# Kernel optimization log

Hardware: AMD Instinct MI355X
Metric: run time of the kernel (lower is better)

## Reference

```python
import jax, jax.numpy as jnp
import numpy as np

# Fixed intrinsics from PhotometricLoss.__init__
W, H = 640, 480
FU, FV = 320.0, 320.0
CU, CV = (W - 1) / 2.0, (H - 1) / 2.0  # cu,cv default to (dim-1)/2
BASELINE = 0.25  # t_vec = [0.25, 0, 0], r_mat = I


def _grid_sample_bilinear_zeros(img, grid):
    """torch.F.grid_sample(img, grid) with bilinear interp, zeros padding,
    align_corners=False (modern torch default).
    img: [B,C,H,W], grid: [B,H,W,2] (x,y) in [-1,1]. Returns [B,C,H,W]."""
    B, C, Hh, Ww = img.shape
    gx, gy = grid[..., 0], grid[..., 1]
    # unnormalize (align_corners=False)
    x = ((gx + 1.0) * Ww - 1.0) * 0.5
    y = ((gy + 1.0) * Hh - 1.0) * 0.5
    x0 = jnp.floor(x)
    y0 = jnp.floor(y)
    wx1 = x - x0
    wy1 = y - y0
    wx0 = 1.0 - wx1
    wy0 = 1.0 - wy1
    b = jnp.arange(B)[:, None, None]

    def gather(yi, xi):
        valid = (xi >= 0) & (xi < Ww) & (yi >= 0) & (yi < Hh)
        xi_c = jnp.clip(xi, 0, Ww - 1).astype(jnp.int32)
        yi_c = jnp.clip(yi, 0, Hh - 1).astype(jnp.int32)
        v = img[b, :, yi_c, xi_c]  # [B,H,W,C]
        return v * valid[..., None].astype(img.dtype)

    out = (gather(y0, x0) * (wy0 * wx0)[..., None]
           + gather(y0, x0 + 1) * (wy0 * wx1)[..., None]
           + gather(y0 + 1, x0) * (wy1 * wx0)[..., None]
           + gather(y0 + 1, x0 + 1) * (wy1 * wx1)[..., None])
    return jnp.transpose(out, (0, 3, 1, 2))  # [B,C,H,W]


def setup_inputs() -> dict:
    key = jax.random.key(0)
    k1, k2, k3 = jax.random.split(key, 3)
    Bsz = 32
    rgb_right = jax.random.uniform(k1, (Bsz, 3, H, W), jnp.float32) * 255.0
    rgb_left = jax.random.uniform(k2, (Bsz, 3, H, W), jnp.float32) * 255.0
    # depth in [1, 80] meters -> disparity fu*B/Z in [1, 80] pixels
    depth_right = jax.random.uniform(k3, (Bsz, 1, H, W), jnp.float32) * 79.0 + 1.0
    return {"rgb_right": rgb_right, "rgb_left": rgb_left, "depth_right": depth_right}


def reference(rgb_right, rgb_left, depth_right):
    # camera rays (X_cam, Y_cam) from Intrinsics
    u = jnp.arange(W, dtype=jnp.float32)
    v = jnp.arange(H, dtype=jnp.float32)
    X_cam = (u[None, :] - CU) / FU  # [1,W] -> broadcasts over H
    Y_cam = (v[:, None] - CV) / FV  # [H,1]

    d = depth_right[:, 0]  # [B,H,W]
    # image_to_pointcloud + transform_curr_to_near (R = I, t = [BASELINE,0,0])
    X = d * X_cam + BASELINE
    Y = d * Y_cam
    Z = jnp.maximum(d, 0.001)  # clamp(min=0.001)

    # pointcloud_to_image
    U_proj = FU * X / Z + CU
    V_proj = FV * Y / Z + CV
    un = 2.0 * U_proj / (W - 1) - 1.0
    vn = 2.0 * V_proj / (H - 1) - 1.0
    un = jnp.where(jnp.abs(un) > 1.0, 2.0, un)  # out-of-frame -> 2 (zeros padding)
    vn = jnp.where(jnp.abs(vn) > 1.0, 2.0, vn)
    grid = jnp.stack([un, vn], axis=-1)  # [B,H,W,2]

    warped = _grid_sample_bilinear_zeros(rgb_left, grid)  # [B,3,H,W]

    diff = jnp.sum(jnp.abs(warped - rgb_right), axis=1)  # [B,H,W]
    valid_mask = ((jnp.sum(warped, axis=1) > 0)
                  & (jnp.sum(rgb_left, axis=1) > 0)).astype(diff.dtype)
    return jnp.mean(diff * valid_mask)
```

## Files before the change

### kernel.cpp

```cpp
#include <hip/hip_runtime.h>

#define IMG_W 640
#define IMG_H 480
#define BATCH 32
#define HWSZ (IMG_H * IMG_W)
#define CHWSZ (3 * HWSZ)
#define NPIX (BATCH * HWSZ)

#define NROWS (BATCH * IMG_H)
#define NTHREADS 320

__global__ __launch_bounds__(NTHREADS) void photo_main(
    const float* __restrict__ rgb_right,
    const float* __restrict__ rgb_left,
    const float* __restrict__ depth,
    float* __restrict__ partials)
{
    const int rowid = blockIdx.x;
    const int b = rowid / IMG_H;
    const int v = rowid - b * IMG_H;

    const float yrow = (480.0f * (float)v) / 479.0f - 0.5f;
    const int y0s = (int)floorf(yrow);
    const int r0 = min(max(y0s, 0), IMG_H - 1);
    const int r1 = min(max(y0s + 1, 0), IMG_H - 1);

    __shared__ float lds[2 * 3 * IMG_W];

    const float* __restrict__ Lb = rgb_left + (size_t)b * CHWSZ;

#pragma unroll
    for (int k = 0; k < 3; ++k) {
        const int idx = threadIdx.x + k * NTHREADS;
        const int rowch = idx / 160;
        const int x4 = idx - rowch * 160;
        const int rowsel = (rowch >= 3) ? 1 : 0;
        const int c = rowch - 3 * rowsel;
        const int rsrc = rowsel ? r1 : r0;
        const float4 val = *(const float4*)(Lb + (size_t)c * HWSZ + (size_t)rsrc * IMG_W + 4 * x4);
        *(float4*)(&lds[rowch * IMG_W + 4 * x4]) = val;
    }
    __syncthreads();

    const size_t dbase = (size_t)b * HWSZ + (size_t)v * IMG_W;
    const size_t rbase = (size_t)b * CHWSZ + (size_t)v * IMG_W;
    const float Yc = ((float)v - 239.5f) * (1.0f / 320.0f);

    float acc = 0.0f;

#pragma unroll
    for (int i = 0; i < 2; ++i) {
        const int u = threadIdx.x + i * NTHREADS;

        const float dd = depth[dbase + u];
        const float Rr = rgb_right[rbase + u];
        const float Rg = rgb_right[rbase + HWSZ + u];
        const float Rb2 = rgb_right[rbase + 2 * HWSZ + u];

        const float Xc = ((float)u - 319.5f) * (1.0f / 320.0f);
        const float X = dd * Xc + 0.25f;
        const float Y = dd * Yc;
        const float Z = fmaxf(dd, 0.001f);
        const float rz = __builtin_amdgcn_rcpf(Z);
        const float Up = 320.0f * X * rz + 319.5f;
        const float Vp = 320.0f * Y * rz + 239.5f;

        float un = 2.0f * Up * (1.0f / 639.0f) - 1.0f;
        float vn = 2.0f * Vp * (1.0f / 479.0f) - 1.0f;
        un = (fabsf(un) > 1.0f) ? 2.0f : un;
        vn = (fabsf(vn) > 1.0f) ? 2.0f : vn;

        const float x = ((un + 1.0f) * (float)IMG_W - 1.0f) * 0.5f;
        const float y = ((vn + 1.0f) * (float)IMG_H - 1.0f) * 0.5f;
        const float x0f = floorf(x);
        const float y0f = floorf(y);
        const float wx1 = x - x0f;
        const float wy1 = y - y0f;
        const float wx0 = 1.0f - wx1;
        const float wy0 = 1.0f - wy1;
        const int x0 = (int)x0f, y0 = (int)y0f;
        const int x1 = x0 + 1,   y1 = y0 + 1;

        const bool vx0 = (x0 >= 0) & (x0 < IMG_W);
        const bool vx1 = (x1 >= 0) & (x1 < IMG_W);
        const bool vy0 = (y0 >= 0) & (y0 < IMG_H);
        const bool vy1 = (y1 >= 0) & (y1 < IMG_H);
        const int cx0 = min(max(x0, 0), IMG_W - 1);
        const int cx1 = min(max(x1, 0), IMG_W - 1);

        const float w00 = wy0 * wx0 * ((vy0 & vx0) ? 1.0f : 0.0f);
        const float w01 = wy0 * wx1 * ((vy0 & vx1) ? 1.0f : 0.0f);
        const float w10 = wy1 * wx0 * ((vy1 & vx0) ? 1.0f : 0.0f);
        const float w11 = wy1 * wx1 * ((vy1 & vx1) ? 1.0f : 0.0f);

        const int s0 = min(max(y0 - y0s, 0), 1) * (3 * IMG_W);
        const int s1 = min(max(y1 - y0s, 0), 1) * (3 * IMG_W);

        float wsum = 0.0f;
        float diff = 0.0f;
#pragma unroll
        for (int c = 0; c < 3; ++c) {
            const int cb = c * IMG_W;
            const float t00 = lds[s0 + cb + cx0];
            const float t01 = lds[s0 + cb + cx1];
            const float t10 = lds[s1 + cb + cx0];
            const float t11 = lds[s1 + cb + cx1];
            const float w = w00 * t00 + w01 * t01 + w10 * t10 + w11 * t11;
            const float r = (c == 0) ? Rr : ((c == 1) ? Rg : Rb2);
            wsum += w;
            diff += fabsf(w - r);
        }

        acc += (wsum > 0.0f) ? diff : 0.0f;
    }

    for (int off = 32; off > 0; off >>= 1)
        acc += __shfl_down(acc, off, 64);

    __shared__ float red[NTHREADS / 64];
    const int lane = threadIdx.x & 63;
    const int wave = threadIdx.x >> 6;
    if (lane == 0) red[wave] = acc;
    __syncthreads();
    if (threadIdx.x == 0) {
        float s = 0.0f;
#pragma unroll
        for (int w = 0; w < NTHREADS / 64; ++w) s += red[w];
        partials[blockIdx.x] = s;
    }
}

__global__ __launch_bounds__(1024) void photo_finish(
    const float* __restrict__ partials,
    float* __restrict__ out,
    int nb)
{
    double s = 0.0;
    for (int i = threadIdx.x; i < nb; i += blockDim.x)
        s += (double)partials[i];

    for (int off = 32; off > 0; off >>= 1)
        s += __shfl_down(s, off, 64);

    __shared__ double lds[16];
    const int lane = threadIdx.x & 63;
    const int wave = threadIdx.x >> 6;
    if (lane == 0) lds[wave] = s;
    __syncthreads();
    if (threadIdx.x == 0) {
        double t = 0.0;
#pragma unroll
        for (int w = 0; w < 16; ++w) t += lds[w];
        out[0] = (float)(t / (double)NPIX);
    }
}

extern "C" void kernel_launch(void* const* d_in, const int* in_sizes, int n_in,
                              void* d_out, int out_size, void* d_ws, size_t ws_size,
                              hipStream_t stream) {
    const float* rgb_right = (const float*)d_in[0];
    const float* rgb_left  = (const float*)d_in[1];
    const float* depth     = (const float*)d_in[2];
    float* partials = (float*)d_ws;
    float* out = (float*)d_out;

    photo_main<<<NROWS, NTHREADS, 0, stream>>>(rgb_right, rgb_left, depth, partials);
    photo_finish<<<1, 1024, 0, stream>>>(partials, out, NROWS);
}
```

Measured before the change: 280.3 us.

## Process two rows per block with shared interleaved-RGB source tile

Each block now handles two output rows with 640 threads and stages three source rows of the left image into shared memory, interleaved as float4 RGB so one LDS load fetches all channels per tap. Because the two output rows share source rows, left-image reads drop from two rows per output row to about 1.5. The projection math is simplified algebraically using the fixed intrinsics: rows map exactly to rows, the vertical coordinate is computed per row, and only the horizontal disparity offset is evaluated. This removes per-pixel vertical bounds logic, but it hardcodes the camera constants and changes the global load pattern to scalar strided loads.

```diff
diff --git a/kernel.cpp b/kernel.cpp
--- a/kernel.cpp
+++ b/kernel.cpp
@@ -7,8 +7,11 @@
 #define CHWSZ (3 * HWSZ)
 #define NPIX (BATCH * HWSZ)
 
-#define NROWS (BATCH * IMG_H)
-#define NTHREADS 320
+#define ROWS_PER_BLK 2
+#define PAIRS_PER_IMG (IMG_H / ROWS_PER_BLK)
+#define NBLOCKS (BATCH * PAIRS_PER_IMG)
+#define NTHREADS IMG_W
+
 
 __global__ __launch_bounds__(NTHREADS) void photo_main(
     const float* __restrict__ rgb_right,
@@ -16,100 +19,81 @@
     const float* __restrict__ depth,
     float* __restrict__ partials)
 {
-    const int rowid = blockIdx.x;
-    const int b = rowid / IMG_H;
-    const int v = rowid - b * IMG_H;
+    const int bb = blockIdx.x / PAIRS_PER_IMG;
+    const int vpair = blockIdx.x - bb * PAIRS_PER_IMG;
+    const int v0 = 2 * vpair;
+    const int t = threadIdx.x;
 
-    const float yrow = (480.0f * (float)v) / 479.0f - 0.5f;
-    const int y0s = (int)floorf(yrow);
-    const int r0 = min(max(y0s, 0), IMG_H - 1);
-    const int r1 = min(max(y0s + 1, 0), IMG_H - 1);
+    __shared__ float4 tile[3 * IMG_W];
+    __shared__ float red[NTHREADS / 64];
 
-    __shared__ float lds[2 * 3 * IMG_W];
+    const float* __restrict__ Lb = rgb_left + (size_t)bb * CHWSZ;
 
-    const float* __restrict__ Lb = rgb_left + (size_t)b * CHWSZ;
+    const float yrow0 = (480.0f * (float)v0) / 479.0f - 0.5f;
+    const int y0s0 = (int)floorf(yrow0);
 
 #pragma unroll
     for (int k = 0; k < 3; ++k) {
-        const int idx = threadIdx.x + k * NTHREADS;
-        const int rowch = idx / 160;
-        const int x4 = idx - rowch * 160;
-        const int rowsel = (rowch >= 3) ? 1 : 0;
-        const int c = rowch - 3 * rowsel;
-        const int rsrc = rowsel ? r1 : r0;
-        const float4 val = *(const float4*)(Lb + (size_t)c * HWSZ + (size_t)rsrc * IMG_W + 4 * x4);
-        *(float4*)(&lds[rowch * IMG_W + 4 * x4]) = val;
+        const int rsrc = min(max(y0s0 + k, 0), IMG_H - 1);
+        const float* src = Lb + (size_t)rsrc * IMG_W + t;
+        tile[k * IMG_W + t] = make_float4(src[0], src[HWSZ], src[2 * HWSZ], 0.0f);
     }
     __syncthreads();
 
-    const size_t dbase = (size_t)b * HWSZ + (size_t)v * IMG_W;
-    const size_t rbase = (size_t)b * CHWSZ + (size_t)v * IMG_W;
-    const float Yc = ((float)v - 239.5f) * (1.0f / 320.0f);
-
+    const float uf = (float)t;
     float acc = 0.0f;
 
 #pragma unroll
-    for (int i = 0; i < 2; ++i) {
-        const int u = threadIdx.x + i * NTHREADS;
+    for (int i = 0; i < ROWS_PER_BLK; ++i) {
+        const int v = v0 + i;
 
-        const float dd = depth[dbase + u];
-        const float Rr = rgb_right[rbase + u];
-        const float Rg = rgb_right[rbase + HWSZ + u];
-        const float Rb2 = rgb_right[rbase + 2 * HWSZ + u];
+        const float yrow = (480.0f * (float)v) / 479.0f - 0.5f;
+        const int y0i = (int)floorf(yrow);
+        const float wy1 = yrow - (float)y0i;
+        const float wy0 = 1.0f - wy1;
+        const float wy0m = (y0i >= 0) ? wy0 : 0.0f;
+        const float wy1m = (y0i + 1 <= IMG_H - 1) ? wy1 : 0.0f;
+        int s0 = min(max(y0i - y0s0, 0), 1);
+        const float4* __restrict__ row0 = &tile[s0 * IMG_W];
+        const float4* __restrict__ row1 = &tile[(s0 + 1) * IMG_W];
 
-        const float Xc = ((float)u - 319.5f) * (1.0f / 320.0f);
-        const float X = dd * Xc + 0.25f;
-        const float Y = dd * Yc;
-        const float Z = fmaxf(dd, 0.001f);
-        const float rz = __builtin_amdgcn_rcpf(Z);
-        const float Up = 320.0f * X * rz + 319.5f;
-        const float Vp = 320.0f * Y * rz + 239.5f;
+        const size_t pbase = (size_t)bb * HWSZ + (size_t)v * IMG_W + t;
+        const size_t cbase = (size_t)bb * CHWSZ + (size_t)v * IMG_W + t;
+        const float dd = depth[pbase];
+        const float Rr = rgb_right[cbase];
+        const float Rg = rgb_right[cbase + HWSZ];
+        const float Rb2 = rgb_right[cbase + 2 * HWSZ];
 
-        float un = 2.0f * Up * (1.0f / 639.0f) - 1.0f;
-        float vn = 2.0f * Vp * (1.0f / 479.0f) - 1.0f;
-        un = (fabsf(un) > 1.0f) ? 2.0f : un;
-        vn = (fabsf(vn) > 1.0f) ? 2.0f : vn;
+        const float rz = __builtin_amdgcn_rcpf(fmaxf(dd, 0.001f));
+        const float Up = fmaf(80.0f, rz, uf);
+        const bool valid = (Up <= 639.0f);
+        const float x = fmaf(Up, 640.0f / 639.0f, -0.5f);
+        const float x0f = floorf(x);
+        const float wx1 = x - x0f;
+        const float wx0 = 1.0f - wx1;
+        const int x0 = (int)x0f;
+        const bool vx1 = (x0 < IMG_W - 1);
+        const int e0 = min(max(x0, 0), IMG_W - 1);
+        const int e1 = min(x0 + 1, IMG_W - 1);
 
-        const float x = ((un + 1.0f) * (float)IMG_W - 1.0f) * 0.5f;
-        const float y = ((vn + 1.0f) * (float)IMG_H - 1.0f) * 0.5f;
-        const float x0f = floorf(x);
-        const float y0f = floorf(y);
-        const float wx1 = x - x0f;
-        const float wy1 = y - y0f;
-        const float wx0 = 1.0f - wx1;
-        const float wy0 = 1.0f - wy1;
-        const int x0 = (int)x0f, y0 = (int)y0f;
-        const int x1 = x0 + 1,   y1 = y0 + 1;
+        const float vm = valid ? 1.0f : 0.0f;
+        const float v1m = (valid && vx1) ? 1.0f : 0.0f;
+        const float w00 = wy0m * wx0 * vm;
+        const float w01 = wy0m * wx1 * v1m;
+        const float w10 = wy1m * wx0 * vm;
+        const float w11 = wy1m * wx1 * v1m;
 
-        const bool vx0 = (x0 >= 0) & (x0 < IMG_W);
-        const bool vx1 = (x1 >= 0) & (x1 < IMG_W);
-        const bool vy0 = (y0 >= 0) & (y0 < IMG_H);
-        const bool vy1 = (y1 >= 0) & (y1 < IMG_H);
-        const int cx0 = min(max(x0, 0), IMG_W - 1);
-        const int cx1 = min(max(x1, 0), IMG_W - 1);
+        const float4 t00 = row0[e0];
+        const float4 t01 = row0[e1];
+        const float4 t10 = row1[e0];
+        const float4 t11 = row1[e1];
 
-        const float w00 = wy0 * wx0 * ((vy0 & vx0) ? 1.0f : 0.0f);
-        const float w01 = wy0 * wx1 * ((vy0 & vx1) ? 1.0f : 0.0f);
-        const float w10 = wy1 * wx0 * ((vy1 & vx0) ? 1.0f : 0.0f);
-        const float w11 = wy1 * wx1 * ((vy1 & vx1) ? 1.0f : 0.0f);
+        const float wa = w00 * t00.x + w01 * t01.x + w10 * t10.x + w11 * t11.x;
+        const float wb = w00 * t00.y + w01 * t01.y + w10 * t10.y + w11 * t11.y;
+        const float wc = w00 * t00.z + w01 * t01.z + w10 * t10.z + w11 * t11.z;
 
-        const int s0 = min(max(y0 - y0s, 0), 1) * (3 * IMG_W);
-        const int s1 = min(max(y1 - y0s, 0), 1) * (3 * IMG_W);
-
-        float wsum = 0.0f;
-        float diff = 0.0f;
-#pragma unroll
-        for (int c = 0; c < 3; ++c) {
-            const int cb = c * IMG_W;
-            const float t00 = lds[s0 + cb + cx0];
-            const float t01 = lds[s0 + cb + cx1];
-            const float t10 = lds[s1 + cb + cx0];
-            const float t11 = lds[s1 + cb + cx1];
-            const float w = w00 * t00 + w01 * t01 + w10 * t10 + w11 * t11;
-            const float r = (c == 0) ? Rr : ((c == 1) ? Rg : Rb2);
-            wsum += w;
-            diff += fabsf(w - r);
-        }
+        const float wsum = wa + wb + wc;
+        const float diff = fabsf(wa - Rr) + fabsf(wb - Rg) + fabsf(wc - Rb2);
 
         acc += (wsum > 0.0f) ? diff : 0.0f;
     }
@@ -117,7 +101,6 @@
     for (int off = 32; off > 0; off >>= 1)
         acc += __shfl_down(acc, off, 64);
 
-    __shared__ float red[NTHREADS / 64];
     const int lane = threadIdx.x & 63;
     const int wave = threadIdx.x >> 6;
     if (lane == 0) red[wave] = acc;
@@ -148,10 +131,10 @@
     if (lane == 0) lds[wave] = s;
     __syncthreads();
     if (threadIdx.x == 0) {
-        double t = 0.0;
+        double tt = 0.0;
 #pragma unroll
-        for (int w = 0; w < 16; ++w) t += lds[w];
-        out[0] = (float)(t / (double)NPIX);
+        for (int w = 0; w < 16; ++w) tt += lds[w];
+        out[0] = (float)(tt / (double)NPIX);
     }
 }
 
@@ -164,6 +147,6 @@
     float* partials = (float*)d_ws;
     float* out = (float*)d_out;
 
-    photo_main<<<NROWS, NTHREADS, 0, stream>>>(rgb_right, rgb_left, depth, partials);
-    photo_finish<<<1, 1024, 0, stream>>>(partials, out, NROWS);
+    photo_main<<<NBLOCKS, NTHREADS, 0, stream>>>(rgb_right, rgb_left, depth, partials);
+    photo_finish<<<1, 1024, 0, stream>>>(partials, out, NBLOCKS);
 }
```

New measurement: 272.3 us. 2.9% less time.
